# Performance work log

Hardware: AMD Instinct MI355X
Metric: run time of the kernel (lower is better)

## Reference

```python
import jax, jax.numpy as jnp
import numpy as np

N_NODES = 100000


def spmm(edge_src, edge_dst, edge_w, h):
    # out[d] = sum_{e: dst[e]=d} w[e] * h[src[e]]  -- sparse adj @ h
    return jax.ops.segment_sum(h[edge_src] * edge_w[:, None], edge_dst,
                               num_segments=N_NODES)


def gcn_layer(x, W, edge_src, edge_dst, edge_w, use_activation):
    support = x @ W                      # dense projection [N, out]
    out = spmm(edge_src, edge_dst, edge_w, support)
    return jax.nn.relu(out) if use_activation else out


def setup_inputs() -> dict:
    key = jax.random.key(0)
    ks = jax.random.split(key, 9)
    n_edges = 3200000

    def xavier(k, shape):
        fan_in, fan_out = shape
        a = jnp.sqrt(6.0 / (fan_in + fan_out))
        return jax.random.uniform(k, shape, jnp.float32, -a, a)

    return {
        "x": jax.random.normal(ks[0], (N_NODES, 512), jnp.float32),
        "edge_src": jax.random.randint(ks[1], (n_edges,), 0, N_NODES, jnp.int32),
        "edge_dst": jax.random.randint(ks[2], (n_edges,), 0, N_NODES, jnp.int32),
        "edge_w": jax.random.uniform(ks[3], (n_edges,), jnp.float32),
        "W1": xavier(ks[4], (512, 128)),
        "W2": xavier(ks[5], (128, 64)),
        "W3": xavier(ks[6], (64, 32)),
        "Wmu": xavier(ks[7], (32, 16)),
        "Wlv": xavier(ks[8], (32, 16)),
    }


def reference(x, edge_src, edge_dst, edge_w, W1, W2, W3, Wmu, Wlv):
    # Eval-mode GCNVAE forward: dropout is identity, z = mu.
    h1 = gcn_layer(x, W1, edge_src, edge_dst, edge_w, True)
    h2 = gcn_layer(h1, W2, edge_src, edge_dst, edge_w, True)
    h3 = gcn_layer(h2, W3, edge_src, edge_dst, edge_w, True)
    mu = gcn_layer(h3, Wmu, edge_src, edge_dst, edge_w, False)
    logvar = gcn_layer(h3, Wlv, edge_src, edge_dst, edge_w, False)
    z = mu  # reparameterize in eval mode returns mu
    return (z, mu, logvar)
```

## Files before the change

kernel.cpp:

```cpp
#include <hip/hip_runtime.h>

typedef __attribute__((ext_vector_type(4))) float floatx4;
typedef __attribute__((ext_vector_type(8))) short bf16x8;

#define NPB 256
#define CHUNK 6144
#define MAXB 12288

__device__ __forceinline__ float bf2f(unsigned short h) {
  union { unsigned int u; float f; } c; c.u = ((unsigned int)h) << 16; return c.f;
}
__device__ __forceinline__ unsigned short f2bf(float f) {
  union { float f; unsigned int u; } c; c.f = f;
  unsigned int r = c.u + 0x7FFFu + ((c.u >> 16) & 1u);
  return (unsigned short)(r >> 16);
}


__global__ __launch_bounds__(256) void bhist_k(const int* __restrict__ dst,
                                               int* __restrict__ bcnt, int E, int B) {
  __shared__ int h[512];
  int tid = threadIdx.x;
  for (int i = tid; i < 512; i += 256) h[i] = 0;
  __syncthreads();
  for (int i = blockIdx.x * 256 + tid; i < E; i += gridDim.x * 256)
    atomicAdd(&h[dst[i] >> 8], 1);
  __syncthreads();
  for (int i = tid; i < B; i += 256)
    if (h[i]) atomicAdd(&bcnt[i], h[i]);
}

__global__ __launch_bounds__(512) void bscan_k(const int* __restrict__ bcnt,
                                               int* __restrict__ bstart,
                                               int* __restrict__ bcur, int B) {
  __shared__ int s[512];
  int tid = threadIdx.x;
  int v = (tid < B) ? bcnt[tid] : 0;
  s[tid] = v;
  __syncthreads();
  for (int off = 1; off < 512; off <<= 1) {
    int t = (tid >= off) ? s[tid - off] : 0;
    __syncthreads();
    s[tid] += t;
    __syncthreads();
  }
  int excl = s[tid] - v;
  if (tid < B) { bstart[tid] = excl; bcur[tid] = excl; }
  if (tid == 511) bstart[B] = s[511];
}

__global__ __launch_bounds__(256) void part_k(const int* __restrict__ src,
                                              const int* __restrict__ dst,
                                              const float* __restrict__ w,
                                              int* __restrict__ bcur,
                                              int2* __restrict__ prec, int E, int B) {
  __shared__ int hist[512];
  __shared__ int lstart[512];
  __shared__ int cur[512];
  __shared__ int gbase[512];
  __shared__ int ss[256];
  __shared__ int2 srt[CHUNK];
  int tid = threadIdx.x;
  int e0 = blockIdx.x * CHUNK;
  int cnt = min(CHUNK, E - e0);
  for (int i = tid; i < 512; i += 256) hist[i] = 0;
  __syncthreads();
  for (int i = tid; i < cnt; i += 256) atomicAdd(&hist[dst[e0 + i] >> 8], 1);
  __syncthreads();
  int a0 = hist[2 * tid], a1 = hist[2 * tid + 1];
  ss[tid] = a0 + a1;
  __syncthreads();
  for (int off = 1; off < 256; off <<= 1) {
    int t = (tid >= off) ? ss[tid - off] : 0;
    __syncthreads();
    ss[tid] += t;
    __syncthreads();
  }
  int excl = tid ? ss[tid - 1] : 0;
  lstart[2 * tid] = excl;     cur[2 * tid] = excl;
  lstart[2 * tid + 1] = excl + a0; cur[2 * tid + 1] = excl + a0;
  __syncthreads();
  for (int i = tid; i < B; i += 256)
    gbase[i] = hist[i] ? atomicAdd(&bcur[i], hist[i]) : 0;
  __syncthreads();
  for (int i = tid; i < cnt; i += 256) {
    int d = dst[e0 + i];
    int b = d >> 8;
    float wf = w[e0 + i];
    int w15 = (int)(wf * 32768.f + 0.5f);
    if (w15 > 32767) w15 = 32767;
    int2 r;
    r.x = src[e0 + i] | (w15 << 17);
    r.y = (b << 8) | (d & 255);
    int pos = atomicAdd(&cur[b], 1);
    srt[pos] = r;
  }
  __syncthreads();
  for (int j = tid; j < cnt; j += 256) {
    int2 r = srt[j];
    int b = r.y >> 8;
    prec[gbase[b] + (j - lstart[b])] = make_int2(r.x, r.y & 255);
  }
}

__global__ __launch_bounds__(256) void sort_k(const int2* __restrict__ prec,
                                              const int* __restrict__ bstart,
                                              unsigned int* __restrict__ recs,
                                              int* __restrict__ row_start,
                                              int* __restrict__ counts, int N, int B) {
  __shared__ int hist[256], lstart[256], cur[256], ss[256];
  __shared__ unsigned int srt[MAXB];
  int b = blockIdx.x;
  int tid = threadIdx.x;
  int s = bstart[b];
  int cnt = bstart[b + 1] - s;
  if (cnt > MAXB) cnt = MAXB;
  hist[tid] = 0;
  __syncthreads();
  for (int i = tid; i < cnt; i += 256) atomicAdd(&hist[prec[s + i].y], 1);
  __syncthreads();
  ss[tid] = hist[tid];
  __syncthreads();
  for (int off = 1; off < 256; off <<= 1) {
    int t = (tid >= off) ? ss[tid - off] : 0;
    __syncthreads();
    ss[tid] += t;
    __syncthreads();
  }
  int excl = ss[tid] - hist[tid];
  lstart[tid] = excl;
  cur[tid] = excl;
  int node = b * NPB + tid;
  if (node < N) { row_start[node] = s + excl; counts[node] = hist[tid]; }
  __syncthreads();
  for (int i = tid; i < cnt; i += 256) {
    int2 r = prec[s + i];
    int pos = atomicAdd(&cur[r.y], 1);
    srt[pos] = (unsigned int)r.x;
  }
  __syncthreads();
  for (int i = tid; i < cnt; i += 256) recs[s + i] = srt[i];
}


__global__ __launch_bounds__(256) void tw1_k(const float* __restrict__ W1,
                                             unsigned short* __restrict__ W1t) {
  int i = blockIdx.x * 256 + threadIdx.x;
  if (i >= 512 * 128) return;
  int k = i >> 7, n = i & 127;
  W1t[n * 512 + k] = f2bf(W1[i]);
}


__global__ __launch_bounds__(256) void gemm1_mfma(const float* __restrict__ A,
                                                  const unsigned short* __restrict__ W1t,
                                                  unsigned short* __restrict__ C, int N) {
  constexpr int K = 512, BK = 64, PAD = 72;
  __shared__ short As[128 * PAD];
  __shared__ short Bs[128 * PAD];
  int tid = threadIdx.x;
  int lane = tid & 63;
  int w = tid >> 6;
  int m0 = lane & 15;
  int kq = lane >> 4;
  int rowBase = blockIdx.x * 128;

  floatx4 acc[8][2];
#pragma unroll
  for (int i = 0; i < 8; ++i)
#pragma unroll
    for (int j = 0; j < 2; ++j) acc[i][j] = (floatx4)0.f;

  for (int k0 = 0; k0 < K; k0 += BK) {
#pragma unroll
    for (int it = 0; it < 8; ++it) {
      int f = (tid + it * 256) * 4;
      int r = f >> 6;
      int kk = f & 63;
      int gr = rowBase + r;
      float4 v = make_float4(0.f, 0.f, 0.f, 0.f);
      if (gr < N) v = *reinterpret_cast<const float4*>(&A[(size_t)gr * K + k0 + kk]);
      unsigned int u0 = ((unsigned int)f2bf(v.y) << 16) | f2bf(v.x);
      unsigned int u1 = ((unsigned int)f2bf(v.w) << 16) | f2bf(v.z);
      *reinterpret_cast<uint2*>(&As[r * PAD + kk]) = make_uint2(u0, u1);
    }
#pragma unroll
    for (int it = 0; it < 4; ++it) {
      int t2 = tid + it * 256;
      int n = t2 >> 3;
      int kc = (t2 & 7) * 8;
      uint4 v = *reinterpret_cast<const uint4*>(&W1t[(size_t)n * 512 + k0 + kc]);
      *reinterpret_cast<uint4*>(&Bs[n * PAD + kc]) = v;
    }
    __syncthreads();
#pragma unroll
    for (int kb = 0; kb < 2; ++kb) {
      int kbase = kb * 32 + kq * 8;
      bf16x8 a[8], bb[2];
#pragma unroll
      for (int mi = 0; mi < 8; ++mi)
        a[mi] = *reinterpret_cast<const bf16x8*>(&As[(mi * 16 + m0) * PAD + kbase]);
#pragma unroll
      for (int jn = 0; jn < 2; ++jn)
        bb[jn] = *reinterpret_cast<const bf16x8*>(&Bs[(w * 32 + jn * 16 + m0) * PAD + kbase]);
#pragma unroll
      for (int mi = 0; mi < 8; ++mi)
#pragma unroll
        for (int jn = 0; jn < 2; ++jn)
          acc[mi][jn] = __builtin_amdgcn_mfma_f32_16x16x32_bf16(a[mi], bb[jn], acc[mi][jn], 0, 0, 0);
    }
    __syncthreads();
  }
#pragma unroll
  for (int mi = 0; mi < 8; ++mi) {
#pragma unroll
    for (int jn = 0; jn < 2; ++jn) {
      int gc = w * 32 + jn * 16 + m0;
#pragma unroll
      for (int p = 0; p < 4; ++p) {
        int gr = rowBase + mi * 16 + kq * 4 + p;
        if (gr < N) C[(size_t)gr * 128 + gc] = f2bf(acc[mi][jn][p]);
      }
    }
  }
}


template <int K, int O>
__global__ __launch_bounds__(256) void gemm_kernel(const unsigned short* __restrict__ A,
                                                   const float* __restrict__ W,
                                                   unsigned short* __restrict__ C, int N) {
  constexpr int BM = 64;
  constexpr int BK = 32;
  constexpr int TM = 4;
  constexpr int TN = O / 16;
  __shared__ float As[BK][BM];
  __shared__ float Ws[BK][O];
  int tid = threadIdx.x;
  int tx = tid % 16;
  int ty = tid / 16;
  int rowBase = blockIdx.x * BM;
  float acc[TM][TN];
#pragma unroll
  for (int i = 0; i < TM; ++i)
#pragma unroll
    for (int j = 0; j < TN; ++j) acc[i][j] = 0.f;

  for (int k0 = 0; k0 < K; k0 += BK) {
    {
      int r = tid >> 2;
      int kc = (tid & 3) * 8;
      int gr = rowBase + r;
      uint4 v = make_uint4(0u, 0u, 0u, 0u);
      if (gr < N) v = *reinterpret_cast<const uint4*>(&A[(size_t)gr * K + k0 + kc]);
      const unsigned short* pv = reinterpret_cast<const unsigned short*>(&v);
#pragma unroll
      for (int j = 0; j < 8; ++j) As[kc + j][r] = bf2f(pv[j]);
    }
    {
      constexpr int ELEMS = BK * O / 256;
      constexpr int NV = ELEMS / 4;
#pragma unroll
      for (int it = 0; it < NV; ++it) {
        int linear = (tid + it * 256) * 4;
        int kk = linear / O;
        int oo = linear % O;
        float4 v = *reinterpret_cast<const float4*>(&W[(size_t)(k0 + kk) * O + oo]);
        Ws[kk][oo + 0] = v.x; Ws[kk][oo + 1] = v.y;
        Ws[kk][oo + 2] = v.z; Ws[kk][oo + 3] = v.w;
      }
    }
    __syncthreads();
#pragma unroll
    for (int k = 0; k < BK; ++k) {
      float a[TM], w[TN];
#pragma unroll
      for (int i = 0; i < TM; ++i) a[i] = As[k][ty * TM + i];
#pragma unroll
      for (int j = 0; j < TN; ++j) w[j] = Ws[k][tx * TN + j];
#pragma unroll
      for (int i = 0; i < TM; ++i)
#pragma unroll
        for (int j = 0; j < TN; ++j) acc[i][j] += a[i] * w[j];
    }
    __syncthreads();
  }
#pragma unroll
  for (int i = 0; i < TM; ++i) {
    int gr = rowBase + ty * TM + i;
    if (gr >= N) continue;
#pragma unroll
    for (int j = 0; j < TN; j += 2) {
      unsigned int p = ((unsigned int)f2bf(acc[i][j + 1]) << 16) | f2bf(acc[i][j]);
      *reinterpret_cast<unsigned int*>(&C[(size_t)gr * O + tx * TN + j]) = p;
    }
  }
}


#define INV32768 3.0517578125e-05f

template <int O, bool RELU>
__global__ __launch_bounds__(256) void spmm_kernel(const unsigned int* __restrict__ recs,
                                                   const int* __restrict__ row_start,
                                                   const int* __restrict__ counts,
                                                   const unsigned short* __restrict__ sup,
                                                   unsigned short* __restrict__ hout, int N) {
  constexpr int SUBW = O / 2;
  constexpr int NPW = 256 / SUBW;
  constexpr int U = 8;
  int tid = threadIdx.x;
  int lane = tid % SUBW;
  int sub = tid / SUBW;
  int node = blockIdx.x * NPW + sub;
  if (node >= N) return;
  int start = row_start[node];
  int deg = counts[node];
  const unsigned int* supu = reinterpret_cast<const unsigned int*>(sup);
  const unsigned int* rp = recs + start;
  float a0 = 0.f, a1 = 0.f;
  int i = 0;
  for (; i + U <= deg; i += U) {
    unsigned int r[U];
#pragma unroll
    for (int j = 0; j < U; ++j) r[j] = rp[i + j];
    unsigned int v[U];
#pragma unroll
    for (int j = 0; j < U; ++j) v[j] = supu[(size_t)(r[j] & 0x1FFFFu) * (O / 2) + lane];
#pragma unroll
    for (int j = 0; j < U; ++j) {
      float w = (float)(r[j] >> 17) * INV32768;
      a0 += w * bf2f((unsigned short)(v[j] & 0xFFFFu));
      a1 += w * bf2f((unsigned short)(v[j] >> 16));
    }
  }
  for (; i < deg; ++i) {
    unsigned int rec = rp[i];
    float w = (float)(rec >> 17) * INV32768;
    unsigned int v = supu[(size_t)(rec & 0x1FFFFu) * (O / 2) + lane];
    a0 += w * bf2f((unsigned short)(v & 0xFFFFu));
    a1 += w * bf2f((unsigned short)(v >> 16));
  }
  if (RELU) { a0 = fmaxf(a0, 0.f); a1 = fmaxf(a1, 0.f); }
  unsigned int p = ((unsigned int)f2bf(a1) << 16) | f2bf(a0);
  reinterpret_cast<unsigned int*>(hout)[(size_t)node * (O / 2) + lane] = p;
}

__global__ __launch_bounds__(256) void spmm_mulv_kernel(const unsigned int* __restrict__ recs,
                                                        const int* __restrict__ row_start,
                                                        const int* __restrict__ counts,
                                                        const unsigned short* __restrict__ sup,
                                                        float* __restrict__ out, int N) {
  constexpr int SUBW = 16;
  constexpr int NPW = 256 / SUBW;
  constexpr int U = 8;
  int tid = threadIdx.x;
  int lane = tid % SUBW;
  int sub = tid / SUBW;
  int node = blockIdx.x * NPW + sub;
  if (node >= N) return;
  int start = row_start[node];
  int deg = counts[node];
  const unsigned int* supu = reinterpret_cast<const unsigned int*>(sup);
  const unsigned int* rp = recs + start;
  float a0 = 0.f, a1 = 0.f;
  int i = 0;
  for (; i + U <= deg; i += U) {
    unsigned int r[U];
#pragma unroll
    for (int j = 0; j < U; ++j) r[j] = rp[i + j];
    unsigned int v[U];
#pragma unroll
    for (int j = 0; j < U; ++j) v[j] = supu[(size_t)(r[j] & 0x1FFFFu) * 16 + lane];
#pragma unroll
    for (int j = 0; j < U; ++j) {
      float w = (float)(r[j] >> 17) * INV32768;
      a0 += w * bf2f((unsigned short)(v[j] & 0xFFFFu));
      a1 += w * bf2f((unsigned short)(v[j] >> 16));
    }
  }
  for (; i < deg; ++i) {
    unsigned int rec = rp[i];
    float w = (float)(rec >> 17) * INV32768;
    unsigned int v = supu[(size_t)(rec & 0x1FFFFu) * 16 + lane];
    a0 += w * bf2f((unsigned short)(v & 0xFFFFu));
    a1 += w * bf2f((unsigned short)(v >> 16));
  }
  size_t nf = (size_t)N * 16;
  if (lane < 8) {
    float2 p = make_float2(a0, a1);
    *reinterpret_cast<float2*>(&out[(size_t)node * 16 + lane * 2]) = p;
    *reinterpret_cast<float2*>(&out[nf + (size_t)node * 16 + lane * 2]) = p;
  } else {
    int l = lane - 8;
    *reinterpret_cast<float2*>(&out[2 * nf + (size_t)node * 16 + l * 2]) =
        make_float2(a0, a1);
  }
}

__global__ void packw_k(const float* __restrict__ Wmu,
                        const float* __restrict__ Wlv,
                        float* __restrict__ Wcat) {
  int i = blockIdx.x * 256 + threadIdx.x;
  if (i >= 32 * 32) return;
  int k = i / 32, o = i % 32;
  Wcat[i] = (o < 16) ? Wmu[k * 16 + o] : Wlv[k * 16 + (o - 16)];
}


extern "C" void kernel_launch(void* const* d_in, const int* in_sizes, int n_in,
                              void* d_out, int out_size, void* d_ws, size_t ws_size,
                              hipStream_t stream) {
  const float* x    = (const float*)d_in[0];
  const int* esrc   = (const int*)d_in[1];
  const int* edst   = (const int*)d_in[2];
  const float* ew   = (const float*)d_in[3];
  const float* W1   = (const float*)d_in[4];
  const float* W2   = (const float*)d_in[5];
  const float* W3   = (const float*)d_in[6];
  const float* Wmu  = (const float*)d_in[7];
  const float* Wlv  = (const float*)d_in[8];
  float* out = (float*)d_out;
  int N = in_sizes[0] / 512;
  int E = in_sizes[1];
  int B = (N + NPB - 1) / NPB;

  char* p = (char*)d_ws;
  auto alloc = [&](size_t bytes) -> char* {
    char* r = p;
    p += (bytes + 255) & ~(size_t)255;
    return r;
  };
  int*  counts = (int*)alloc((size_t)N * 4);
  int*  rowst  = (int*)alloc((size_t)N * 4);
  int*  bcnt   = (int*)alloc((size_t)(B + 1) * 4);
  int*  bstart = (int*)alloc((size_t)(B + 1) * 4);
  int*  bcur   = (int*)alloc((size_t)(B + 1) * 4);
  int2* prec   = (int2*)alloc((size_t)E * 8);
  unsigned int* recs = (unsigned int*)alloc((size_t)E * 4);
  unsigned short* bufA = (unsigned short*)alloc((size_t)N * 128 * 2);
  unsigned short* bufB = (unsigned short*)alloc((size_t)N * 128 * 2);
  unsigned short* W1t  = (unsigned short*)alloc(512 * 128 * 2);
  float* Wcat = (float*)alloc(32 * 32 * 4);

  hipMemsetAsync(bcnt, 0, (size_t)(B + 1) * 4, stream);
  bhist_k<<<256, 256, 0, stream>>>(edst, bcnt, E, B);
  bscan_k<<<1, 512, 0, stream>>>(bcnt, bstart, bcur, B);
  part_k<<<(E + CHUNK - 1) / CHUNK, 256, 0, stream>>>(esrc, edst, ew, bcur, prec, E, B);
  sort_k<<<B, 256, 0, stream>>>(prec, bstart, recs, rowst, counts, N, B);

  tw1_k<<<256, 256, 0, stream>>>(W1, W1t);
  gemm1_mfma<<<(N + 127) / 128, 256, 0, stream>>>(x, W1t, bufA, N);
  spmm_kernel<128, true><<<(N + 3) / 4, 256, 0, stream>>>(recs, rowst, counts, bufA, bufB, N);

  int gemmGrid = (N + 63) / 64;

  gemm_kernel<128, 64><<<gemmGrid, 256, 0, stream>>>(bufB, W2, bufA, N);
  spmm_kernel<64, true><<<(N + 7) / 8, 256, 0, stream>>>(recs, rowst, counts, bufA, bufB, N);

  gemm_kernel<64, 32><<<gemmGrid, 256, 0, stream>>>(bufB, W3, bufA, N);
  spmm_kernel<32, true><<<(N + 15) / 16, 256, 0, stream>>>(recs, rowst, counts, bufA, bufB, N);

  packw_k<<<4, 256, 0, stream>>>(Wmu, Wlv, Wcat);
  gemm_kernel<32, 32><<<gemmGrid, 256, 0, stream>>>(bufB, Wcat, bufA, N);
  spmm_mulv_kernel<<<(N + 15) / 16, 256, 0, stream>>>(recs, rowst, counts, bufA, out, N);
}
```

Baseline: 795.8 us.

## Double-buffer gemm1 with direct global-to-LDS loads and swizzled fp32 tiles

Rewrites the first-layer GEMM to stage A (fp32) and W1t tiles straight into LDS with global_load_lds, double-buffered with BK=32, so the next tile's loads overlap the current tile's MFMAs. The fp32-to-bf16 conversion moves from the store path to the read path, and an XOR swizzle on the A tile is meant to avoid LDS bank conflicts. Occupancy is hinted to 3 blocks per CU. In exchange, LDS use per stage doubles for A because it stays fp32, each element gets converted once per wave that reads it, and the raw vmcnt waits make correctness depend on the exact count of outstanding loads.

Result: faster. 770.2 us (-3.2%).

```diff
diff --git a/kernel.cpp b/kernel.cpp
--- a/kernel.cpp
+++ b/kernel.cpp
@@ -14,6 +14,12 @@
   union { float f; unsigned int u; } c; c.f = f;
   unsigned int r = c.u + 0x7FFFu + ((c.u >> 16) & 1u);
   return (unsigned short)(r >> 16);
+}
+
+__device__ __forceinline__ void gl16(const void* g, void* l) {
+  __builtin_amdgcn_global_load_lds(
+      (const __attribute__((address_space(1))) unsigned int*)g,
+      (__attribute__((address_space(3))) unsigned int*)l, 16, 0, 0);
 }
 
 
@@ -152,12 +158,21 @@
 }
 
 
-__global__ __launch_bounds__(256) void gemm1_mfma(const float* __restrict__ A,
-                                                  const unsigned short* __restrict__ W1t,
-                                                  unsigned short* __restrict__ C, int N) {
-  constexpr int K = 512, BK = 64, PAD = 72;
-  __shared__ short As[128 * PAD];
-  __shared__ short Bs[128 * PAD];
+__device__ __forceinline__ bf16x8 cvt8(float4 lo, float4 hi) {
+  bf16x8 r;
+  r[0] = (short)f2bf(lo.x); r[1] = (short)f2bf(lo.y);
+  r[2] = (short)f2bf(lo.z); r[3] = (short)f2bf(lo.w);
+  r[4] = (short)f2bf(hi.x); r[5] = (short)f2bf(hi.y);
+  r[6] = (short)f2bf(hi.z); r[7] = (short)f2bf(hi.w);
+  return r;
+}
+
+__global__ __launch_bounds__(256, 3) void gemm1_mfma(const float* __restrict__ A,
+                                                     const unsigned short* __restrict__ W1t,
+                                                     unsigned short* __restrict__ C, int N) {
+  constexpr int BK = 32;
+  __shared__ __align__(16) float          As[2][128 * BK];
+  __shared__ __align__(16) unsigned short Bs[2][128 * BK];
   int tid = threadIdx.x;
   int lane = tid & 63;
   int w = tid >> 6;
@@ -171,46 +186,60 @@
 #pragma unroll
     for (int j = 0; j < 2; ++j) acc[i][j] = (floatx4)0.f;
 
-  for (int k0 = 0; k0 < K; k0 += BK) {
-#pragma unroll
-    for (int it = 0; it < 8; ++it) {
-      int f = (tid + it * 256) * 4;
-      int r = f >> 6;
-      int kk = f & 63;
-      int gr = rowBase + r;
-      float4 v = make_float4(0.f, 0.f, 0.f, 0.f);
-      if (gr < N) v = *reinterpret_cast<const float4*>(&A[(size_t)gr * K + k0 + kk]);
-      unsigned int u0 = ((unsigned int)f2bf(v.y) << 16) | f2bf(v.x);
-      unsigned int u1 = ((unsigned int)f2bf(v.w) << 16) | f2bf(v.z);
-      *reinterpret_cast<uint2*>(&As[r * PAD + kk]) = make_uint2(u0, u1);
-    }
-#pragma unroll
-    for (int it = 0; it < 4; ++it) {
-      int t2 = tid + it * 256;
-      int n = t2 >> 3;
-      int kc = (t2 & 7) * 8;
-      uint4 v = *reinterpret_cast<const uint4*>(&W1t[(size_t)n * 512 + k0 + kc]);
-      *reinterpret_cast<uint4*>(&Bs[n * PAD + kc]) = v;
-    }
-    __syncthreads();
-#pragma unroll
-    for (int kb = 0; kb < 2; ++kb) {
-      int kbase = kb * 32 + kq * 8;
-      bf16x8 a[8], bb[2];
-#pragma unroll
-      for (int mi = 0; mi < 8; ++mi)
-        a[mi] = *reinterpret_cast<const bf16x8*>(&As[(mi * 16 + m0) * PAD + kbase]);
-#pragma unroll
-      for (int jn = 0; jn < 2; ++jn)
-        bb[jn] = *reinterpret_cast<const bf16x8*>(&Bs[(w * 32 + jn * 16 + m0) * PAD + kbase]);
-#pragma unroll
-      for (int mi = 0; mi < 8; ++mi)
-#pragma unroll
-        for (int jn = 0; jn < 2; ++jn)
-          acc[mi][jn] = __builtin_amdgcn_mfma_f32_16x16x32_bf16(a[mi], bb[jn], acc[mi][jn], 0, 0, 0);
-    }
-    __syncthreads();
-  }
+  size_t aSrc[4]; int aDst[4];
+#pragma unroll
+  for (int it = 0; it < 4; ++it) {
+    int c = it * 256 + w * 64 + lane;
+    int r = c >> 3, ch = c & 7;
+    int sc = ch ^ (r & 7);
+    int gr = rowBase + r;
+    if (gr > N - 1) gr = N - 1;
+    aSrc[it] = (size_t)gr * 512 + sc * 4;
+    aDst[it] = (it * 256 + w * 64) * 4;
+  }
+  size_t bSrc[2]; int bDst[2];
+#pragma unroll
+  for (int it = 0; it < 2; ++it) {
+    int c = it * 256 + w * 64 + lane;
+    int n = c >> 2, ch = c & 3;
+    bSrc[it] = (size_t)n * 512 + ch * 8;
+    bDst[it] = (it * 256 + w * 64) * 8;
+  }
+
+  auto stage = [&](int bi, int k0) {
+#pragma unroll
+    for (int it = 0; it < 4; ++it) gl16(&A[aSrc[it] + k0], &As[bi][aDst[it]]);
+#pragma unroll
+    for (int it = 0; it < 2; ++it) gl16(&W1t[bSrc[it] + k0], &Bs[bi][bDst[it]]);
+  };
+
+  stage(0, 0);
+  int cur = 0;
+  for (int t = 0; t < 16; ++t) {
+    if (t < 15) {
+      stage(cur ^ 1, (t + 1) * BK);
+      asm volatile("s_waitcnt vmcnt(6)" ::: "memory");
+    } else {
+      asm volatile("s_waitcnt vmcnt(0)" ::: "memory");
+    }
+    __builtin_amdgcn_s_barrier();
+
+    bf16x8 bb0 = *reinterpret_cast<const bf16x8*>(&Bs[cur][(w * 32 + m0) * BK + kq * 8]);
+    bf16x8 bb1 = *reinterpret_cast<const bf16x8*>(&Bs[cur][(w * 32 + 16 + m0) * BK + kq * 8]);
+#pragma unroll
+    for (int mi = 0; mi < 8; ++mi) {
+      int row = mi * 16 + m0;
+      int s = row & 7;
+      float4 lo = *reinterpret_cast<const float4*>(&As[cur][row * BK + (((2 * kq) ^ s) << 2)]);
+      float4 hi = *reinterpret_cast<const float4*>(&As[cur][row * BK + (((2 * kq + 1) ^ s) << 2)]);
+      bf16x8 a = cvt8(lo, hi);
+      acc[mi][0] = __builtin_amdgcn_mfma_f32_16x16x32_bf16(a, bb0, acc[mi][0], 0, 0, 0);
+      acc[mi][1] = __builtin_amdgcn_mfma_f32_16x16x32_bf16(a, bb1, acc[mi][1], 0, 0, 0);
+    }
+    __builtin_amdgcn_s_barrier();
+    cur ^= 1;
+  }
+
 #pragma unroll
   for (int mi = 0; mi < 8; ++mi) {
 #pragma unroll
```
